# Kernel optimization log

Measured on AMD Instinct MI355X. Metric: run time of the kernel, lower is better.

Reference implementation:

```python
import jax, jax.numpy as jnp
import numpy as np

NEG_SLOPE = 0.2


def gat_layer(x, adj, W, a_src, a_dst):
    # x: (C, in_dim), adj: (C, C) 0/1, W: (in_dim, H*D), a_src/a_dst: (H, D)
    C = x.shape[0]
    H, D = a_src.shape
    h = (x @ W).reshape(C, H, D)            # (C, H, D)
    hh = jnp.transpose(h, (1, 0, 2))        # (H, C, D)
    asrc = jnp.einsum('hcd,hd->hc', hh, a_src)  # (H, C)
    adst = jnp.einsum('hcd,hd->hc', hh, a_dst)  # (H, C)
    e = asrc[:, :, None] + adst[:, None, :]     # (H, C, C)
    e = jax.nn.leaky_relu(e, NEG_SLOPE)
    e = jnp.where(adj[None, :, :] == 0, -jnp.inf, e)
    attn = jax.nn.softmax(e, axis=-1)           # (H, C, C)
    out = jnp.einsum('hij,hjd->hid', attn, hh)  # (H, C, D)
    return jnp.transpose(out, (1, 0, 2)).reshape(C, H * D)


def setup_inputs() -> dict:
    key = jax.random.key(0)
    ks = jax.random.split(key, 12)
    B, doc_dim = 1024, 768
    C, label_dim = 4096, 768
    hidden, H = 512, 4
    D = hidden // H  # 128

    doc_x = jax.random.normal(ks[0], (B, doc_dim), dtype=jnp.float32)
    label_init = jax.random.normal(ks[1], (C, label_dim), dtype=jnp.float32)
    adj = jax.random.randint(ks[2], (C, C), 0, 2, dtype=jnp.int32)
    adj = adj.at[jnp.arange(C), jnp.arange(C)].set(1)  # self-loops

    def xavier(k, shape):
        fan_in, fan_out = shape[0], shape[1]
        lim = jnp.sqrt(6.0 / (fan_in + fan_out)).astype(jnp.float32)
        return jax.random.uniform(k, shape, jnp.float32, -lim, lim)

    W1 = xavier(ks[3], (label_dim, hidden))
    a_src1 = xavier(ks[4], (H, D))
    a_dst1 = xavier(ks[5], (H, D))
    W2 = xavier(ks[6], (hidden, hidden))
    a_src2 = xavier(ks[7], (H, D))
    a_dst2 = xavier(ks[8], (H, D))
    Wd = xavier(ks[9], (doc_dim, hidden))
    bd = jnp.zeros((hidden,), jnp.float32)
    return {"doc_x": doc_x, "label_init": label_init, "adj": adj,
            "W1": W1, "a_src1": a_src1, "a_dst1": a_dst1,
            "W2": W2, "a_src2": a_src2, "a_dst2": a_dst2,
            "Wd": Wd, "bd": bd}


def reference(doc_x, label_init, adj, W1, a_src1, a_dst1, W2, a_src2, a_dst2, Wd, bd):
    # doc_proj (dropout = identity in eval)
    doc_h = jax.nn.relu(doc_x @ Wd + bd)            # (B, hidden)
    # label encoder: GAT -> ELU -> GAT
    h = gat_layer(label_init, adj, W1, a_src1, a_dst1)
    h = jax.nn.elu(h)
    label_h = gat_layer(h, adj, W2, a_src2, a_dst2)  # (C, hidden)
    logits = doc_h @ label_h.T                      # (B, C)
    return logits
```

## Files before the change

kernel.cpp:

```cpp
#include <hip/hip_runtime.h>
#include <hip/hip_bf16.h>
#include <math.h>

#define BDOCS   1024
#define CNODES  4096
#define INDIM   768
#define HID     512
#define NHEAD   4
#define HDIM    128
#define NEG_SLOPE 0.2f

#define KSPLIT  8
#define JPER    (CNODES / KSPLIT)
#define NCH     (JPER / 32)

typedef __attribute__((ext_vector_type(8))) short short8;
typedef __attribute__((ext_vector_type(4))) float f32x4;

__device__ __forceinline__ float lrelu(float x) { return x > 0.f ? x : NEG_SLOPE * x; }

__device__ __forceinline__ short f2bf(float f) {
    union { float f; unsigned u; } v; v.f = f;
    unsigned r = (v.u + 0x7fff + ((v.u >> 16) & 1)) >> 16;
    return (short)r;
}
__device__ __forceinline__ float bf2f(short s) {
    union { float f; unsigned u; } v; v.u = ((unsigned)(unsigned short)s) << 16;
    return v.f;
}
__device__ __forceinline__ unsigned pk2(float a, float b) {
    union { float f; unsigned u; } x, y; x.f = a; y.f = b;
    unsigned lo = (x.u + 0x7fff + ((x.u >> 16) & 1)) >> 16;
    unsigned hi = (y.u + 0x7fff + ((y.u >> 16) & 1)) >> 16;
    return lo | (hi << 16);
}
__device__ __forceinline__ short hup(float f) {
    union { float f; unsigned u; } v; v.f = f;
    return (short)((v.u + 0x8000) >> 16);
}

__global__ __launch_bounds__(256)
void pack_adj(const int* __restrict__ adj, unsigned long long* __restrict__ adjb64)
{
    const int t    = threadIdx.x;
    const int gw   = blockIdx.x * 4 + (t >> 6);
    const int lane = t & 63;
    const int i  = gw >> 6;
    const int j0 = (gw & 63) * 64;
    const int a  = adj[(size_t)i * CNODES + j0 + lane];
    const unsigned long long m = __ballot(a != 0);
    if (lane == 0) adjb64[(size_t)i * 64 + (j0 >> 6)] = m;
}

__global__ __launch_bounds__(256)
void frag_T(const float* __restrict__ src, short* __restrict__ dst, int N, int K)
{
    __shared__ float tile[32][132];
    const int jc = blockIdx.x;
    const int nq = blockIdx.y;
    const int t  = threadIdx.x;
    const int KC = K >> 5;
#pragma unroll
    for (int it = 0; it < 16; it++) {
        const int e = it * 256 + t;
        const int j = e >> 7, n = e & 127;
        tile[j][n] = src[(size_t)(jc * 32 + j) * N + nq * 128 + n];
    }
    __syncthreads();
#pragma unroll
    for (int s = 0; s < 2; s++) {
        const int item = s * 256 + t;
        const int nbl = item >> 6, lane = item & 63;
        const int nr = lane & 15, kq = lane >> 4;
        short8 v;
#pragma unroll
        for (int jr = 0; jr < 8; jr++)
            v[jr] = f2bf(tile[kq * 8 + jr][nbl * 16 + nr]);
        *(short8*)&dst[((size_t)((nq * 8 + nbl) * KC + jc) * 64 + lane) * 8] = v;
    }
}

__global__ __launch_bounds__(256)
void frag_A(const float* __restrict__ src, short* __restrict__ dst, int C)
{
    __shared__ float tile[16][132];
    const int rb = blockIdx.x, cq = blockIdx.y;
    const int t  = threadIdx.x;
    const int KC = C >> 5;
#pragma unroll
    for (int it = 0; it < 8; it++) {
        const int e = it * 256 + t;
        const int r = e >> 7, c = e & 127;
        tile[r][c] = src[(size_t)(rb * 16 + r) * C + cq * 128 + c];
    }
    __syncthreads();
    const int kcl = t >> 6, lane = t & 63;
    const int m = lane & 15, kq = lane >> 4;
    short8 v8;
#pragma unroll
    for (int j = 0; j < 8; j++) v8[j] = f2bf(tile[m][kcl * 32 + kq * 8 + j]);
    *(short8*)&dst[((size_t)(rb * KC + cq * 4 + kcl) * 64 + lane) * 8] = v8;
}

template <int KC>
__global__ __launch_bounds__(64)
void gemm_hpre(const short* __restrict__ Af, const short* __restrict__ Bf,
               const float* __restrict__ a_src, const float* __restrict__ a_dst,
               short* __restrict__ hbTf, float* __restrict__ asrc, float* __restrict__ adst)
{
    __shared__ __align__(16) short tileT[128][24];
    const int lane = threadIdx.x;
    const int mb   = blockIdx.x;
    const int nq   = blockIdx.y;
    const int i0   = mb * 16;

    f32x4 acc[8];
#pragma unroll
    for (int c = 0; c < 8; c++) acc[c] = (f32x4){0.f, 0.f, 0.f, 0.f};

    const short* ap = Af + (size_t)mb * KC * 512 + lane * 8;
    const short* bp = Bf + (size_t)(nq * 8) * KC * 512 + lane * 8;

#pragma unroll 2
    for (int kc = 0; kc < KC; kc++) {
        short8 a = *(const short8*)(ap + (size_t)kc * 512);
#pragma unroll
        for (int c = 0; c < 8; c++) {
            short8 bf = *(const short8*)(bp + ((size_t)c * KC + kc) * 512);
            acc[c] = __builtin_amdgcn_mfma_f32_16x16x32_bf16(a, bf, acc[c], 0, 0, 0);
        }
    }

    const int col = lane & 15, q4 = lane >> 4;

#pragma unroll
    for (int c = 0; c < 8; c++) {
        uint2 u;
        u.x = pk2(acc[c][0], acc[c][1]);
        u.y = pk2(acc[c][2], acc[c][3]);
        *(uint2*)&tileT[c * 16 + col][q4 * 4] = u;
    }
    __syncthreads();
    {
        const int jc = mb >> 1, khalf = mb & 1;
        const int nr = lane & 15, kq = lane >> 4;
        if ((kq >> 1) == khalf) {
#pragma unroll
            for (int nbl = 0; nbl < 8; nbl++) {
                short8 v = *(const short8*)&tileT[nbl * 16 + nr][(kq & 1) * 8];
                *(short8*)&hbTf[(((size_t)(nq * 8 + nbl) * (CNODES / 32) + jc) * 64 + lane) * 8] = v;
            }
        }
    }

    float ssrc[4] = {}, sdst[4] = {};
#pragma unroll
    for (int c = 0; c < 8; c++) {
        const float vs = a_src[nq * 128 + c * 16 + col];
        const float vd = a_dst[nq * 128 + c * 16 + col];
#pragma unroll
        for (int r = 0; r < 4; r++) {
            ssrc[r] += acc[c][r] * vs;
            sdst[r] += acc[c][r] * vd;
        }
    }
#pragma unroll
    for (int mask = 1; mask <= 8; mask <<= 1)
#pragma unroll
        for (int r = 0; r < 4; r++) {
            ssrc[r] += __shfl_xor(ssrc[r], mask);
            sdst[r] += __shfl_xor(sdst[r], mask);
        }
    if (col == 0) {
#pragma unroll
        for (int r = 0; r < 4; r++) {
            const int row = i0 + q4 * 4 + r;
            asrc[nq * CNODES + row] = ssrc[r];
            adst[nq * CNODES + row] = sdst[r];
        }
    }
}

template <int KC>
__global__ __launch_bounds__(64)
void gemm_doc(const short* __restrict__ Af, const short* __restrict__ Bf,
              const float* __restrict__ bias, short* __restrict__ dhf)
{
    __shared__ __align__(16) short tile[16][64];
    const int lane = threadIdx.x;
    const int mb = blockIdx.x;
    const int ng = blockIdx.y;

    f32x4 acc[4];
#pragma unroll
    for (int c = 0; c < 4; c++) acc[c] = (f32x4){0.f, 0.f, 0.f, 0.f};

    const short* ap = Af + (size_t)mb * KC * 512 + lane * 8;
    const short* bp = Bf + (size_t)(ng * 4) * KC * 512 + lane * 8;

#pragma unroll 2
    for (int kc = 0; kc < KC; kc++) {
        short8 a = *(const short8*)(ap + (size_t)kc * 512);
#pragma unroll
        for (int c = 0; c < 4; c++) {
            short8 bf = *(const short8*)(bp + ((size_t)c * KC + kc) * 512);
            acc[c] = __builtin_amdgcn_mfma_f32_16x16x32_bf16(a, bf, acc[c], 0, 0, 0);
        }
    }

    const int col = lane & 15, q4 = lane >> 4;
#pragma unroll
    for (int c = 0; c < 4; c++)
#pragma unroll
        for (int r = 0; r < 4; r++) {
            float v = fmaxf(acc[c][r] + bias[ng * 64 + c * 16 + col], 0.f);
            tile[q4 * 4 + r][c * 16 + col] = f2bf(v);
        }
    __syncthreads();
    const int m = lane & 15, kq = lane >> 4;
#pragma unroll
    for (int kcl = 0; kcl < 2; kcl++) {
        short8 v = *(const short8*)&tile[m][kcl * 32 + kq * 8];
        *(short8*)&dhf[(((size_t)mb * 16 + ng * 2 + kcl) * 64 + lane) * 8] = v;
    }
}

template <int KC>
__global__ __launch_bounds__(64)
void gemm_frag(const short* __restrict__ Af, const short* __restrict__ Bf,
               float* __restrict__ Cmat, int N)
{
    const int lane = threadIdx.x;
    const int mb0  = blockIdx.x * 2;
    const int nq   = blockIdx.y;

    f32x4 acc[2][8];
#pragma unroll
    for (int f = 0; f < 2; f++)
#pragma unroll
        for (int c = 0; c < 8; c++) acc[f][c] = (f32x4){0.f, 0.f, 0.f, 0.f};

    const short* ap0 = Af + (size_t)mb0 * KC * 512 + lane * 8;
    const short* ap1 = ap0 + (size_t)KC * 512;
    const short* bp  = Bf + (size_t)(nq * 8) * KC * 512 + lane * 8;

#pragma unroll 2
    for (int kc = 0; kc < KC; kc++) {
        short8 a0 = *(const short8*)(ap0 + (size_t)kc * 512);
        short8 a1 = *(const short8*)(ap1 + (size_t)kc * 512);
        short8 bf[8];
#pragma unroll
        for (int c = 0; c < 8; c++)
            bf[c] = *(const short8*)(bp + ((size_t)c * KC + kc) * 512);
#pragma unroll
        for (int c = 0; c < 8; c++) {
            acc[0][c] = __builtin_amdgcn_mfma_f32_16x16x32_bf16(a0, bf[c], acc[0][c], 0, 0, 0);
            acc[1][c] = __builtin_amdgcn_mfma_f32_16x16x32_bf16(a1, bf[c], acc[1][c], 0, 0, 0);
        }
    }

    const int col = lane & 15, q4 = lane >> 4;
#pragma unroll
    for (int f = 0; f < 2; f++)
#pragma unroll
        for (int c = 0; c < 8; c++)
#pragma unroll
            for (int r = 0; r < 4; r++) {
                const int row = (mb0 + f) * 16 + q4 * 4 + r;
                Cmat[(size_t)row * N + nq * 128 + c * 16 + col] = acc[f][c][r];
            }
}

__global__ __launch_bounds__(1024)
void stats_exp(const float* __restrict__ adst, float* __restrict__ Mh,
               float* __restrict__ E1, float* __restrict__ E2)
{
    __shared__ float red[1024];
    __shared__ float s_mh;
    const int h = blockIdx.x, t = threadIdx.x;
    const float4 d4 = *(const float4*)(adst + (size_t)h * CNODES + t * 4);
    float m = fmaxf(fmaxf(d4.x, d4.y), fmaxf(d4.z, d4.w));
    red[t] = m; __syncthreads();
    for (int s = 512; s >= 1; s >>= 1) {
        if (t < s) red[t] = fmaxf(red[t], red[t + s]);
        __syncthreads();
    }
    if (t == 0) { s_mh = red[0]; Mh[h] = red[0]; }
    __syncthreads();
    const float mh = s_mh;
    float4 e1, e2;
    e1.x = __expf(d4.x - mh); e2.x = __expf(0.2f * (d4.x - mh));
    e1.y = __expf(d4.y - mh); e2.y = __expf(0.2f * (d4.y - mh));
    e1.z = __expf(d4.z - mh); e2.z = __expf(0.2f * (d4.z - mh));
    e1.w = __expf(d4.w - mh); e2.w = __expf(0.2f * (d4.w - mh));
    *(float4*)(E1 + (size_t)h * CNODES + t * 4) = e1;
    *(float4*)(E2 + (size_t)h * CNODES + t * 4) = e2;
}

__global__ __launch_bounds__(256, 3)
void attn_pv(const short* __restrict__ hbTf,
             const unsigned int* __restrict__ adjb,
             const float* __restrict__ asrc,
             const float* __restrict__ E1, const float* __restrict__ E2,
             const float* __restrict__ Mh,
             short* __restrict__ part, float* __restrict__ lpart)
{
    __shared__ __align__(16) short tileO[32][520];
    const int t    = threadIdx.x;
    const int w    = t >> 6;
    const int lane = t & 63;
    const int m    = lane & 15;
    const int kq   = lane >> 4;
    const int i0   = blockIdx.x * 32;
    const int ks   = blockIdx.y;
    const int js   = ks * JPER;

    const float mh  = Mh[w];
    const float as0 = asrc[w * CNODES + i0 + m];
    const float as1 = asrc[w * CNODES + i0 + 16 + m];
    const float mr0 = lrelu(as0 + mh), mr1 = lrelu(as1 + mh);
    const float A10 = __expf(as0 + mh - mr0),          A11 = __expf(as1 + mh - mr1);
    const float A20 = __expf(0.2f * (as0 + mh) - mr0), A21 = __expf(0.2f * (as1 + mh) - mr1);
    const float T00 = __expf(-as0 - mh),               T01 = __expf(-as1 - mh);

    f32x4 acc[2][8], accO[2];
#pragma unroll
    for (int f = 0; f < 2; f++) {
        accO[f] = (f32x4){0.f, 0.f, 0.f, 0.f};
#pragma unroll
        for (int c = 0; c < 8; c++) acc[f][c] = (f32x4){0.f, 0.f, 0.f, 0.f};
    }
    short8 ones;
#pragma unroll
    for (int q = 0; q < 8; q++) ones[q] = (short)0x3F80;

    const unsigned int* ar0 = adjb + (size_t)(i0 + m) * 128 + ks * NCH;
    const unsigned int* ar1 = adjb + (size_t)(i0 + 16 + m) * 128 + ks * NCH;

#pragma unroll 2
    for (int ch = 0; ch < NCH; ch++) {
        const int j0 = js + ch * 32;
        const unsigned int aw0 = ar0[ch] >> (kq * 8);
        const unsigned int aw1 = ar1[ch] >> (kq * 8);
        const float4* p1 = (const float4*)(E1 + (size_t)w * CNODES + j0 + kq * 8);
        const float4* p2 = (const float4*)(E2 + (size_t)w * CNODES + j0 + kq * 8);
        const float4 x0 = p1[0], x1 = p1[1];
        const float4 y0 = p2[0], y1 = p2[1];
        const float e1v[8] = {x0.x, x0.y, x0.z, x0.w, x1.x, x1.y, x1.z, x1.w};
        const float e2v[8] = {y0.x, y0.y, y0.z, y0.w, y1.x, y1.y, y1.z, y1.w};

        short8 bf[8];
        const short* bbase = hbTf + (((size_t)(w * 8) * 128 + (j0 >> 5)) * 64 + lane) * 8;
#pragma unroll
        for (int c = 0; c < 8; c++)
            bf[c] = *(const short8*)(bbase + (size_t)c * 128 * 64 * 8);

        short8 a0, a1;
#pragma unroll
        for (int q = 0; q < 8; q++) {
            const float e1 = e1v[q], e2 = e2v[q];
            const bool c0 = e1 > T00, c1 = e1 > T01;
            float w0 = (c0 ? A10 : A20) * (c0 ? e1 : e2);
            float w1 = (c1 ? A11 : A21) * (c1 ? e1 : e2);
            w0 = ((aw0 >> q) & 1u) ? w0 : 0.f;
            w1 = ((aw1 >> q) & 1u) ? w1 : 0.f;
            a0[q] = hup(w0);
            a1[q] = hup(w1);
        }

#pragma unroll
        for (int c = 0; c < 8; c++) {
            acc[0][c] = __builtin_amdgcn_mfma_f32_16x16x32_bf16(a0, bf[c], acc[0][c], 0, 0, 0);
            acc[1][c] = __builtin_amdgcn_mfma_f32_16x16x32_bf16(a1, bf[c], acc[1][c], 0, 0, 0);
        }
        accO[0] = __builtin_amdgcn_mfma_f32_16x16x32_bf16(a0, ones, accO[0], 0, 0, 0);
        accO[1] = __builtin_amdgcn_mfma_f32_16x16x32_bf16(a1, ones, accO[1], 0, 0, 0);
    }

    const int col = lane & 15, q4 = lane >> 4;
    if (m == 0) {
#pragma unroll
        for (int f = 0; f < 2; f++)
#pragma unroll
            for (int r = 0; r < 4; r++)
                lpart[((size_t)ks * NHEAD + w) * CNODES + i0 + f * 16 + q4 * 4 + r] = accO[f][r];
    }

#pragma unroll
    for (int f = 0; f < 2; f++)
#pragma unroll
        for (int c = 0; c < 8; c++)
#pragma unroll
            for (int r = 0; r < 4; r++)
                tileO[f * 16 + q4 * 4 + r][w * 128 + c * 16 + col] = f2bf(acc[f][c][r]);
    __syncthreads();
    short* pS = part + (size_t)ks * CNODES * HID;
#pragma unroll
    for (int it = 0; it < 8; it++) {
        const int u   = it * 256 + t;
        const int row = u >> 6, un = u & 63;
        uint4 v = *(const uint4*)&tileO[row][un * 8];
        *(uint4*)&pS[(size_t)(i0 + row) * HID + un * 8] = v;
    }
}

template <bool ELU>
__global__ __launch_bounds__(256)
void reduce_norm_frag(const short* __restrict__ part, const float* __restrict__ lpart,
                      short* __restrict__ dst)
{
    const int t = threadIdx.x;
    const int W = blockIdx.x * 4 + (t >> 6);
    const int lane = t & 63;
    const int rb = W >> 4, kc = W & 15;
    const int m = lane & 15, kq = lane >> 4;
    const int i = rb * 16 + m;
    const int n0 = kc * 32 + kq * 8;
    const int h = kc >> 2;

    float v[8] = {};
    float l = 0.f;
#pragma unroll
    for (int s = 0; s < KSPLIT; s++) {
        const uint4 raw = *(const uint4*)&part[(size_t)s * CNODES * HID + (size_t)i * HID + n0];
        const unsigned rr[4] = {raw.x, raw.y, raw.z, raw.w};
#pragma unroll
        for (int q = 0; q < 4; q++) {
            v[q * 2]     += bf2f((short)(rr[q] & 0xffff));
            v[q * 2 + 1] += bf2f((short)(rr[q] >> 16));
        }
        l += lpart[((size_t)s * NHEAD + h) * CNODES + i];
    }
    const float inv = 1.0f / l;
    short8 o;
#pragma unroll
    for (int q = 0; q < 8; q++) {
        float x = v[q] * inv;
        if (ELU) x = x > 0.f ? x : (__expf(x) - 1.f);
        o[q] = f2bf(x);
    }
    *(short8*)&dst[((size_t)(rb * 16 + kc) * 64 + lane) * 8] = o;
}

extern "C" void kernel_launch(void* const* d_in, const int* in_sizes, int n_in,
                              void* d_out, int out_size, void* d_ws, size_t ws_size,
                              hipStream_t stream)
{
    const float* doc_x      = (const float*)d_in[0];
    const float* label_init = (const float*)d_in[1];
    const int*   adj        = (const int*)d_in[2];
    const float* W1         = (const float*)d_in[3];
    const float* a_src1     = (const float*)d_in[4];
    const float* a_dst1     = (const float*)d_in[5];
    const float* W2         = (const float*)d_in[6];
    const float* a_src2     = (const float*)d_in[7];
    const float* a_dst2     = (const float*)d_in[8];
    const float* Wd         = (const float*)d_in[9];
    const float* bd         = (const float*)d_in[10];
    float*       out        = (float*)d_out;

    char* wsb = (char*)d_ws;
    size_t off = 0;
    auto alloc = [&](size_t bytes) -> char* {
        char* p = wsb + off;
        off = (off + bytes + 255) & ~(size_t)255;
        return p;
    };

    float* asrc  = (float*)alloc(NHEAD * CNODES * 4);
    float* adst  = (float*)alloc(NHEAD * CNODES * 4);
    float* Mh    = (float*)alloc(256);
    float* E1    = (float*)alloc(NHEAD * CNODES * 4);
    float* E2    = (float*)alloc(NHEAD * CNODES * 4);
    float* lpart = (float*)alloc((size_t)KSPLIT * NHEAD * CNODES * 4);
    unsigned int* adjb = (unsigned int*)alloc((size_t)CNODES * 128 * 4);
    short* hbTf  = (short*)alloc((size_t)CNODES * HID * 2);
    short* Wdf   = (short*)alloc((size_t)INDIM * HID * 2);
    short* W1f   = (short*)alloc((size_t)INDIM * HID * 2);
    short* W2f   = (short*)alloc((size_t)HID * HID * 2);
    short* dxf   = (short*)alloc((size_t)BDOCS * INDIM * 2);
    short* Af_li = (short*)alloc((size_t)CNODES * INDIM * 2);
    short* Af2   = (short*)alloc((size_t)CNODES * HID * 2);
    short* lhf   = (short*)alloc((size_t)CNODES * HID * 2);
    short* dhf   = (short*)alloc((size_t)BDOCS * HID * 2);
    short* part  = (short*)alloc((size_t)KSPLIT * CNODES * HID * 2);
    (void)ws_size;

    const dim3 blk(256);

    pack_adj<<<CNODES * CNODES / 64 / 4, blk, 0, stream>>>(adj, (unsigned long long*)adjb);
    frag_T<<<dim3(INDIM / 32, HID / 128), blk, 0, stream>>>(Wd, Wdf, HID, INDIM);
    frag_T<<<dim3(INDIM / 32, HID / 128), blk, 0, stream>>>(W1, W1f, HID, INDIM);
    frag_T<<<dim3(HID / 32, HID / 128), blk, 0, stream>>>(W2, W2f, HID, HID);
    frag_A<<<dim3(BDOCS / 16, INDIM / 128), blk, 0, stream>>>(doc_x, dxf, INDIM);
    frag_A<<<dim3(CNODES / 16, INDIM / 128), blk, 0, stream>>>(label_init, Af_li, INDIM);

    gemm_doc<INDIM / 32><<<dim3(BDOCS / 16, HID / 64), 64, 0, stream>>>(dxf, Wdf, bd, dhf);

    gemm_hpre<INDIM / 32><<<dim3(CNODES / 16, NHEAD), 64, 0, stream>>>(
        Af_li, W1f, a_src1, a_dst1, hbTf, asrc, adst);

    stats_exp<<<NHEAD, 1024, 0, stream>>>(adst, Mh, E1, E2);
    attn_pv<<<dim3(CNODES / 32, KSPLIT), blk, 0, stream>>>(hbTf, adjb, asrc, E1, E2, Mh, part, lpart);
    reduce_norm_frag<true><<<CNODES * HID / 256 / 8, blk, 0, stream>>>(part, lpart, Af2);

    gemm_hpre<HID / 32><<<dim3(CNODES / 16, NHEAD), 64, 0, stream>>>(
        Af2, W2f, a_src2, a_dst2, hbTf, asrc, adst);

    stats_exp<<<NHEAD, 1024, 0, stream>>>(adst, Mh, E1, E2);
    attn_pv<<<dim3(CNODES / 32, KSPLIT), blk, 0, stream>>>(hbTf, adjb, asrc, E1, E2, Mh, part, lpart);
    reduce_norm_frag<false><<<CNODES * HID / 256 / 8, blk, 0, stream>>>(part, lpart, lhf);

    gemm_frag<HID / 32><<<dim3(BDOCS / 32, CNODES / 128), 64, 0, stream>>>(dhf, lhf, out, CNODES);
}
```

Baseline: 381.0 us.

## Enlarge attn_pv row tile to 64 and merge prep kernels into one launch

The attention-PV kernel now handles 64 query rows per block instead of 32, so each loaded hbTf B-fragment feeds four MFMA row groups, and adjacency bits are fetched as uint4 for four chunks at once. Output is staged through shared memory in two halves. The six preprocessing kernels (adjacency bit-packing and bf16 fragment conversions) are merged into one launch to cut launch overhead, and gemm_frag loads B fragments inside the MFMA loop. The larger accumulator set raises register pressure, so occupancy drops from 3 to 2 blocks per SIMD-bound and the grid halves, which risks poorer latency hiding.

```diff
diff --git a/kernel.cpp b/kernel.cpp
--- a/kernel.cpp
+++ b/kernel.cpp
@@ -39,25 +39,9 @@
     return (short)((v.u + 0x8000) >> 16);
 }
 
-__global__ __launch_bounds__(256)
-void pack_adj(const int* __restrict__ adj, unsigned long long* __restrict__ adjb64)
-{
-    const int t    = threadIdx.x;
-    const int gw   = blockIdx.x * 4 + (t >> 6);
-    const int lane = t & 63;
-    const int i  = gw >> 6;
-    const int j0 = (gw & 63) * 64;
-    const int a  = adj[(size_t)i * CNODES + j0 + lane];
-    const unsigned long long m = __ballot(a != 0);
-    if (lane == 0) adjb64[(size_t)i * 64 + (j0 >> 6)] = m;
-}
-
-__global__ __launch_bounds__(256)
-void frag_T(const float* __restrict__ src, short* __restrict__ dst, int N, int K)
-{
-    __shared__ float tile[32][132];
-    const int jc = blockIdx.x;
-    const int nq = blockIdx.y;
+__device__ void frag_T_dev(const float* __restrict__ src, short* __restrict__ dst,
+                           int N, int K, int jc, int nq, float (*tile)[132])
+{
     const int t  = threadIdx.x;
     const int KC = K >> 5;
 #pragma unroll
@@ -80,11 +64,9 @@
     }
 }
 
-__global__ __launch_bounds__(256)
-void frag_A(const float* __restrict__ src, short* __restrict__ dst, int C)
-{
-    __shared__ float tile[16][132];
-    const int rb = blockIdx.x, cq = blockIdx.y;
+__device__ void frag_A_dev(const float* __restrict__ src, short* __restrict__ dst,
+                           int C, int rb, int cq, float (*tile)[132])
+{
     const int t  = threadIdx.x;
     const int KC = C >> 5;
 #pragma unroll
@@ -100,6 +82,40 @@
 #pragma unroll
     for (int j = 0; j < 8; j++) v8[j] = f2bf(tile[m][kcl * 32 + kq * 8 + j]);
     *(short8*)&dst[((size_t)(rb * KC + cq * 4 + kcl) * 64 + lane) * 8] = v8;
+}
+
+#define PREP_BLOCKS (65536 + 96 + 96 + 64 + 384 + 1536)
+__global__ __launch_bounds__(256)
+void prep_all(const int* __restrict__ adj, unsigned long long* __restrict__ adjb64,
+              const float* __restrict__ Wd, short* __restrict__ Wdf,
+              const float* __restrict__ W1, short* __restrict__ W1f,
+              const float* __restrict__ W2, short* __restrict__ W2f,
+              const float* __restrict__ doc_x, short* __restrict__ dxf,
+              const float* __restrict__ label_init, short* __restrict__ lif)
+{
+    __shared__ float tile[32][132];
+    int b = blockIdx.x;
+    if (b < 65536) {
+        const int t    = threadIdx.x;
+        const int gw   = b * 4 + (t >> 6);
+        const int lane = t & 63;
+        const int i  = gw >> 6;
+        const int j0 = (gw & 63) * 64;
+        const int a  = adj[(size_t)i * CNODES + j0 + lane];
+        const unsigned long long msk = __ballot(a != 0);
+        if (lane == 0) adjb64[(size_t)i * 64 + (j0 >> 6)] = msk;
+        return;
+    }
+    b -= 65536;
+    if (b < 96)  { frag_T_dev(Wd, Wdf, HID, INDIM, b % 24, b / 24, tile); return; }
+    b -= 96;
+    if (b < 96)  { frag_T_dev(W1, W1f, HID, INDIM, b % 24, b / 24, tile); return; }
+    b -= 96;
+    if (b < 64)  { frag_T_dev(W2, W2f, HID, HID, b % 16, b / 16, tile); return; }
+    b -= 64;
+    if (b < 384) { frag_A_dev(doc_x, dxf, INDIM, b % 64, b / 64, tile); return; }
+    b -= 384;
+    frag_A_dev(label_init, lif, INDIM, b % 256, b / 256, tile);
 }
 
 template <int KC>
@@ -248,14 +264,11 @@
     for (int kc = 0; kc < KC; kc++) {
         short8 a0 = *(const short8*)(ap0 + (size_t)kc * 512);
         short8 a1 = *(const short8*)(ap1 + (size_t)kc * 512);
-        short8 bf[8];
-#pragma unroll
-        for (int c = 0; c < 8; c++)
-            bf[c] = *(const short8*)(bp + ((size_t)c * KC + kc) * 512);
 #pragma unroll
         for (int c = 0; c < 8; c++) {
-            acc[0][c] = __builtin_amdgcn_mfma_f32_16x16x32_bf16(a0, bf[c], acc[0][c], 0, 0, 0);
-            acc[1][c] = __builtin_amdgcn_mfma_f32_16x16x32_bf16(a1, bf[c], acc[1][c], 0, 0, 0);
+            short8 bf = *(const short8*)(bp + ((size_t)c * KC + kc) * 512);
+            acc[0][c] = __builtin_amdgcn_mfma_f32_16x16x32_bf16(a0, bf, acc[0][c], 0, 0, 0);
+            acc[1][c] = __builtin_amdgcn_mfma_f32_16x16x32_bf16(a1, bf, acc[1][c], 0, 0, 0);
         }
     }
 
@@ -297,7 +310,7 @@
     *(float4*)(E2 + (size_t)h * CNODES + t * 4) = e2;
 }
 
-__global__ __launch_bounds__(256, 3)
+__global__ __launch_bounds__(256, 2)
 void attn_pv(const short* __restrict__ hbTf,
              const unsigned int* __restrict__ adjb,
              const float* __restrict__ asrc,
@@ -311,96 +324,108 @@
     const int lane = t & 63;
     const int m    = lane & 15;
     const int kq   = lane >> 4;
-    const int i0   = blockIdx.x * 32;
+    const int i0   = blockIdx.x * 64;
     const int ks   = blockIdx.y;
     const int js   = ks * JPER;
 
-    const float mh  = Mh[w];
-    const float as0 = asrc[w * CNODES + i0 + m];
-    const float as1 = asrc[w * CNODES + i0 + 16 + m];
-    const float mr0 = lrelu(as0 + mh), mr1 = lrelu(as1 + mh);
-    const float A10 = __expf(as0 + mh - mr0),          A11 = __expf(as1 + mh - mr1);
-    const float A20 = __expf(0.2f * (as0 + mh) - mr0), A21 = __expf(0.2f * (as1 + mh) - mr1);
-    const float T00 = __expf(-as0 - mh),               T01 = __expf(-as1 - mh);
-
-    f32x4 acc[2][8], accO[2];
-#pragma unroll
-    for (int f = 0; f < 2; f++) {
-        accO[f] = (f32x4){0.f, 0.f, 0.f, 0.f};
-#pragma unroll
-        for (int c = 0; c < 8; c++) acc[f][c] = (f32x4){0.f, 0.f, 0.f, 0.f};
+    const float mh = Mh[w];
+    float A1[4], A2[4], T0[4];
+#pragma unroll
+    for (int g = 0; g < 4; g++) {
+        const float as = asrc[w * CNODES + i0 + g * 16 + m];
+        const float mr = lrelu(as + mh);
+        A1[g] = __expf(as + mh - mr);
+        A2[g] = __expf(0.2f * (as + mh) - mr);
+        T0[g] = __expf(-as - mh);
+    }
+
+    f32x4 acc[4][8], accO[4];
+#pragma unroll
+    for (int g = 0; g < 4; g++) {
+        accO[g] = (f32x4){0.f, 0.f, 0.f, 0.f};
+#pragma unroll
+        for (int c = 0; c < 8; c++) acc[g][c] = (f32x4){0.f, 0.f, 0.f, 0.f};
     }
     short8 ones;
 #pragma unroll
     for (int q = 0; q < 8; q++) ones[q] = (short)0x3F80;
 
-    const unsigned int* ar0 = adjb + (size_t)(i0 + m) * 128 + ks * NCH;
-    const unsigned int* ar1 = adjb + (size_t)(i0 + 16 + m) * 128 + ks * NCH;
-
-#pragma unroll 2
-    for (int ch = 0; ch < NCH; ch++) {
-        const int j0 = js + ch * 32;
-        const unsigned int aw0 = ar0[ch] >> (kq * 8);
-        const unsigned int aw1 = ar1[ch] >> (kq * 8);
-        const float4* p1 = (const float4*)(E1 + (size_t)w * CNODES + j0 + kq * 8);
-        const float4* p2 = (const float4*)(E2 + (size_t)w * CNODES + j0 + kq * 8);
-        const float4 x0 = p1[0], x1 = p1[1];
-        const float4 y0 = p2[0], y1 = p2[1];
-        const float e1v[8] = {x0.x, x0.y, x0.z, x0.w, x1.x, x1.y, x1.z, x1.w};
-        const float e2v[8] = {y0.x, y0.y, y0.z, y0.w, y1.x, y1.y, y1.z, y1.w};
-
-        short8 bf[8];
-        const short* bbase = hbTf + (((size_t)(w * 8) * 128 + (j0 >> 5)) * 64 + lane) * 8;
-#pragma unroll
-        for (int c = 0; c < 8; c++)
-            bf[c] = *(const short8*)(bbase + (size_t)c * 128 * 64 * 8);
-
-        short8 a0, a1;
-#pragma unroll
-        for (int q = 0; q < 8; q++) {
-            const float e1 = e1v[q], e2 = e2v[q];
-            const bool c0 = e1 > T00, c1 = e1 > T01;
-            float w0 = (c0 ? A10 : A20) * (c0 ? e1 : e2);
-            float w1 = (c1 ? A11 : A21) * (c1 ? e1 : e2);
-            w0 = ((aw0 >> q) & 1u) ? w0 : 0.f;
-            w1 = ((aw1 >> q) & 1u) ? w1 : 0.f;
-            a0[q] = hup(w0);
-            a1[q] = hup(w1);
-        }
-
-#pragma unroll
-        for (int c = 0; c < 8; c++) {
-            acc[0][c] = __builtin_amdgcn_mfma_f32_16x16x32_bf16(a0, bf[c], acc[0][c], 0, 0, 0);
-            acc[1][c] = __builtin_amdgcn_mfma_f32_16x16x32_bf16(a1, bf[c], acc[1][c], 0, 0, 0);
-        }
-        accO[0] = __builtin_amdgcn_mfma_f32_16x16x32_bf16(a0, ones, accO[0], 0, 0, 0);
-        accO[1] = __builtin_amdgcn_mfma_f32_16x16x32_bf16(a1, ones, accO[1], 0, 0, 0);
-    }
-
-    const int col = lane & 15, q4 = lane >> 4;
+    for (int ch4 = 0; ch4 < 4; ch4++) {
+        uint4 am[4];
+#pragma unroll
+        for (int g = 0; g < 4; g++)
+            am[g] = *(const uint4*)(adjb + (size_t)(i0 + g * 16 + m) * 128 + ks * NCH + ch4 * 4);
+
+#pragma unroll
+        for (int chi = 0; chi < 4; chi++) {
+            const int j0 = js + (ch4 * 4 + chi) * 32;
+            unsigned aw[4];
+#pragma unroll
+            for (int g = 0; g < 4; g++)
+                aw[g] = ((const unsigned*)&am[g])[chi] >> (kq * 8);
+
+            const float4* p1 = (const float4*)(E1 + (size_t)w * CNODES + j0 + kq * 8);
+            const float4* p2 = (const float4*)(E2 + (size_t)w * CNODES + j0 + kq * 8);
+            const float4 x0 = p1[0], x1 = p1[1];
+            const float4 y0 = p2[0], y1 = p2[1];
+            const float e1v[8] = {x0.x, x0.y, x0.z, x0.w, x1.x, x1.y, x1.z, x1.w};
+            const float e2v[8] = {y0.x, y0.y, y0.z, y0.w, y1.x, y1.y, y1.z, y1.w};
+
+            short8 a[4];
+#pragma unroll
+            for (int q = 0; q < 8; q++) {
+                const float e1 = e1v[q], e2 = e2v[q];
+#pragma unroll
+                for (int g = 0; g < 4; g++) {
+                    const bool c0 = e1 > T0[g];
+                    float wv = (c0 ? A1[g] : A2[g]) * (c0 ? e1 : e2);
+                    wv = ((aw[g] >> q) & 1u) ? wv : 0.f;
+                    a[g][q] = hup(wv);
+                }
+            }
+
+            const short* bbase = hbTf + (((size_t)(w * 8) * 128 + (j0 >> 5)) * 64 + lane) * 8;
+#pragma unroll
+            for (int c = 0; c < 8; c++) {
+                short8 bf = *(const short8*)(bbase + (size_t)c * 128 * 64 * 8);
+                acc[0][c] = __builtin_amdgcn_mfma_f32_16x16x32_bf16(a[0], bf, acc[0][c], 0, 0, 0);
+                acc[1][c] = __builtin_amdgcn_mfma_f32_16x16x32_bf16(a[1], bf, acc[1][c], 0, 0, 0);
+                acc[2][c] = __builtin_amdgcn_mfma_f32_16x16x32_bf16(a[2], bf, acc[2][c], 0, 0, 0);
+                acc[3][c] = __builtin_amdgcn_mfma_f32_16x16x32_bf16(a[3], bf, acc[3][c], 0, 0, 0);
+            }
+#pragma unroll
+            for (int g = 0; g < 4; g++)
+                accO[g] = __builtin_amdgcn_mfma_f32_16x16x32_bf16(a[g], ones, accO[g], 0, 0, 0);
+        }
+    }
+
+    const int col = m, q4 = kq;
     if (m == 0) {
 #pragma unroll
+        for (int g = 0; g < 4; g++)
+#pragma unroll
+            for (int r = 0; r < 4; r++)
+                lpart[((size_t)ks * NHEAD + w) * CNODES + i0 + g * 16 + q4 * 4 + r] = accO[g][r];
+    }
+
+    short* pS = part + (size_t)ks * CNODES * HID;
+    for (int half = 0; half < 2; half++) {
+        __syncthreads();
+#pragma unroll
         for (int f = 0; f < 2; f++)
 #pragma unroll
-            for (int r = 0; r < 4; r++)
-                lpart[((size_t)ks * NHEAD + w) * CNODES + i0 + f * 16 + q4 * 4 + r] = accO[f][r];
-    }
-
-#pragma unroll
-    for (int f = 0; f < 2; f++)
-#pragma unroll
-        for (int c = 0; c < 8; c++)
-#pragma unroll
-            for (int r = 0; r < 4; r++)
-                tileO[f * 16 + q4 * 4 + r][w * 128 + c * 16 + col] = f2bf(acc[f][c][r]);
-    __syncthreads();
-    short* pS = part + (size_t)ks * CNODES * HID;
-#pragma unroll
-    for (int it = 0; it < 8; it++) {
-        const int u   = it * 256 + t;
-        const int row = u >> 6, un = u & 63;
-        uint4 v = *(const uint4*)&tileO[row][un * 8];
-        *(uint4*)&pS[(size_t)(i0 + row) * HID + un * 8] = v;
+            for (int c = 0; c < 8; c++)
+#pragma unroll
+                for (int r = 0; r < 4; r++)
+                    tileO[f * 16 + q4 * 4 + r][w * 128 + c * 16 + col] = f2bf(acc[half * 2 + f][c][r]);
+        __syncthreads();
+#pragma unroll
+        for (int it = 0; it < 8; it++) {
+            const int u   = it * 256 + t;
+            const int row = u >> 6, un = u & 63;
+            uint4 v = *(const uint4*)&tileO[row][un * 8];
+            *(uint4*)&pS[(size_t)(i0 + half * 32 + row) * HID + un * 8] = v;
+        }
     }
 }
 
@@ -488,12 +513,9 @@
 
     const dim3 blk(256);
 
-    pack_adj<<<CNODES * CNODES / 64 / 4, blk, 0, stream>>>(adj, (unsigned long long*)adjb);
-    frag_T<<<dim3(INDIM / 32, HID / 128), blk, 0, stream>>>(Wd, Wdf, HID, INDIM);
-    frag_T<<<dim3(INDIM / 32, HID / 128), blk, 0, stream>>>(W1, W1f, HID, INDIM);
-    frag_T<<<dim3(HID / 32, HID / 128), blk, 0, stream>>>(W2, W2f, HID, HID);
-    frag_A<<<dim3(BDOCS / 16, INDIM / 128), blk, 0, stream>>>(doc_x, dxf, INDIM);
-    frag_A<<<dim3(CNODES / 16, INDIM / 128), blk, 0, stream>>>(label_init, Af_li, INDIM);
+    prep_all<<<PREP_BLOCKS, blk, 0, stream>>>(adj, (unsigned long long*)adjb,
+                                              Wd, Wdf, W1, W1f, W2, W2f,
+                                              doc_x, dxf, label_init, Af_li);
 
     gemm_doc<INDIM / 32><<<dim3(BDOCS / 16, HID / 64), 64, 0, stream>>>(dxf, Wdf, bd, dhf);
 
@@ -501,14 +523,14 @@
         Af_li, W1f, a_src1, a_dst1, hbTf, asrc, adst);
 
     stats_exp<<<NHEAD, 1024, 0, stream>>>(adst, Mh, E1, E2);
-    attn_pv<<<dim3(CNODES / 32, KSPLIT), blk, 0, stream>>>(hbTf, adjb, asrc, E1, E2, Mh, part, lpart);
+    attn_pv<<<dim3(CNODES / 64, KSPLIT), blk, 0, stream>>>(hbTf, adjb, asrc, E1, E2, Mh, part, lpart);
     reduce_norm_frag<true><<<CNODES * HID / 256 / 8, blk, 0, stream>>>(part, lpart, Af2);
 
     gemm_hpre<HID / 32><<<dim3(CNODES / 16, NHEAD), 64, 0, stream>>>(
         Af2, W2f, a_src2, a_dst2, hbTf, asrc, adst);
 
     stats_exp<<<NHEAD, 1024, 0, stream>>>(adst, Mh, E1, E2);
-    attn_pv<<<dim3(CNODES / 32, KSPLIT), blk, 0, stream>>>(hbTf, adjb, asrc, E1, E2, Mh, part, lpart);
+    attn_pv<<<dim3(CNODES / 64, KSPLIT), blk, 0, stream>>>(hbTf, adjb, asrc, E1, E2, Mh, part, lpart);
     reduce_norm_frag<false><<<CNODES * HID / 256 / 8, blk, 0, stream>>>(part, lpart, lhf);
 
     gemm_frag<HID / 32><<<dim3(BDOCS / 32, CNODES / 128), 64, 0, stream>>>(dhf, lhf, out, CNODES);
```

Result: slower. 400.5 us (+5.1%).
